# Kernel tuning notes

Measured on AMD Instinct MI355X. Metric: run time of the kernel, lower is better.

Reference implementation:

```python
import jax, jax.numpy as jnp
import numpy as np

H_GRU = 32  # GRU hidden size fixed to 32 in the module


def setup_inputs() -> dict:
    key = jax.random.key(0)
    ks = jax.random.split(key, 12)
    B, C_in, H, W = 64, 64, 48, 160
    C_out = 64
    s_in = 1.0 / np.sqrt(C_in)
    s_h = 1.0 / np.sqrt(H_GRU)
    u = lambda k, shape: jax.random.uniform(k, shape, jnp.float32, -s_h, s_h)
    return {
        "x": jax.random.normal(ks[0], (B, C_in, H, W), jnp.float32),
        "conv_w": jax.random.normal(ks[1], (C_out, C_in), jnp.float32) * s_in,
        "conv_b": jax.random.normal(ks[2], (C_out,), jnp.float32) * s_in,
        "wih_f": u(ks[3], (3 * H_GRU, C_out)),
        "whh_f": u(ks[4], (3 * H_GRU, H_GRU)),
        "bih_f": u(ks[5], (3 * H_GRU,)),
        "bhh_f": u(ks[6], (3 * H_GRU,)),
        "wih_b": u(ks[7], (3 * H_GRU, C_out)),
        "whh_b": u(ks[8], (3 * H_GRU, H_GRU)),
        "bih_b": u(ks[9], (3 * H_GRU,)),
        "bhh_b": u(ks[10], (3 * H_GRU,)),
    }


def _gru_scan(pre, whh, bhh):
    # pre: [N, T, 3H] input-side gate pre-activations (already x@Wih^T + bih)
    N = pre.shape[0]

    def step(h, g):
        gh = h @ whh.T + bhh
        gi_r, gi_z, gi_n = jnp.split(g, 3, axis=-1)
        gh_r, gh_z, gh_n = jnp.split(gh, 3, axis=-1)
        r = jax.nn.sigmoid(gi_r + gh_r)
        z = jax.nn.sigmoid(gi_z + gh_z)
        n = jnp.tanh(gi_n + r * gh_n)
        h_new = (1.0 - z) * n + z * h
        return h_new, h_new

    h0 = jnp.zeros((N, H_GRU), pre.dtype)
    _, ys = jax.lax.scan(step, h0, jnp.swapaxes(pre, 0, 1))  # ys: [T, N, H]
    return jnp.swapaxes(ys, 0, 1)  # [N, T, H]


def reference(x, conv_w, conv_b, wih_f, whh_f, bih_f, bhh_f,
              wih_b, whh_b, bih_b, bhh_b):
    B, C_in, H, W = x.shape
    # 1x1 conv fused with the NCHW->NHWC permute
    y = jnp.einsum('bchw,oc->bhwo', x, conv_w) + conv_b  # [B, H, W, C_out]
    C_out = y.shape[-1]
    seq = y.reshape(B * H, W, C_out)  # GRU batch = B*H, seq_len = W
    # forward direction
    pre_f = jnp.einsum('ntc,gc->ntg', seq, wih_f) + bih_f
    out_f = _gru_scan(pre_f, whh_f, bhh_f)
    # backward direction: scan reversed sequence, then flip output back
    seq_r = seq[:, ::-1, :]
    pre_b = jnp.einsum('ntc,gc->ntg', seq_r, wih_b) + bih_b
    out_b = _gru_scan(pre_b, whh_b, bhh_b)[:, ::-1, :]
    out = jnp.concatenate([out_f, out_b], axis=-1)  # [B*H, W, 2*H_GRU]
    out = out.reshape(B, H, W, 2 * H_GRU)
    return jnp.transpose(out, (0, 3, 1, 2))  # back to NCHW
```

## Files before the change

### kernel.cpp

```cpp
#include <hip/hip_runtime.h>


typedef _Float16 f16x8 __attribute__((ext_vector_type(8)));
typedef _Float16 f16x4 __attribute__((ext_vector_type(4)));
typedef __fp16   pk16  __attribute__((ext_vector_type(2)));
typedef float    f32x4 __attribute__((ext_vector_type(4)));

#define HWSTRIDE 7680
#define NW 10
#define WS_WHH2_OFF 24576
#define WS_BIAS_OFF 36864

__global__ void fold_weights(const float* __restrict__ conv_w,
                             const float* __restrict__ conv_b,
                             const float* __restrict__ wih_f,
                             const float* __restrict__ bih_f,
                             const float* __restrict__ bhh_f,
                             const float* __restrict__ wih_b,
                             const float* __restrict__ bih_b,
                             const float* __restrict__ bhh_b,
                             const float* __restrict__ whh_f,
                             const float* __restrict__ whh_b,
                             void* wsv)
{
    _Float16* W2   = (_Float16*)wsv;
    _Float16* whh2 = (_Float16*)((char*)wsv + WS_WHH2_OFF);
    float*    bias = (float*)((char*)wsv + WS_BIAS_OFF);
    const int idx = blockIdx.x * 256 + threadIdx.x;
    if (idx < 12288) {
        const int d = idx / 6144, r = idx % 6144, g = r / 64, c = r % 64;
        const float* wih = d ? wih_b : wih_f;
        float acc = 0.f;
        for (int o = 0; o < 64; ++o) acc += wih[g * 64 + o] * conv_w[o * 64 + c];
        W2[idx] = (_Float16)acc;
    } else if (idx < 18432) {
        const int e2 = idx - 12288;
        const int dd = e2 / 3072, rr = e2 % 3072, g = rr / 32, k = rr % 32;
        const int qq = k >> 3, ee = k & 7;
        const int jsrc = (ee < 4) ? (qq * 4 + ee) : (16 + qq * 4 + (ee - 4));
        const float* whh = dd ? whh_b : whh_f;
        whh2[e2] = (_Float16)whh[g * 32 + jsrc];
    } else if (idx < 18688) {
        const int e = idx - 18432;
        const int d = e >> 7, rr = e & 127, kind = rr >> 5, j = rr & 31;
        const float* wih = d ? wih_b : wih_f;
        const float* bih = d ? bih_b : bih_f;
        const float* bhh = d ? bhh_b : bhh_f;
        float v;
        if (kind == 0 || kind == 1) {
            const int g = j + kind * 32;
            float b2 = bih[g];
            for (int o = 0; o < 64; ++o) b2 += wih[g * 64 + o] * conv_b[o];
            v = b2 + bhh[g];
        } else if (kind == 2) {
            const int g = j + 64;
            float b2 = bih[g];
            for (int o = 0; o < 64; ++o) b2 += wih[g * 64 + o] * conv_b[o];
            v = b2;
        } else {
            v = bhh[j + 64];
        }
        bias[(d * 4 + kind) * 32 + j] = v;
    }
}

static __device__ __forceinline__ unsigned pkh(float a, float b) {
    pk16 p = __builtin_amdgcn_cvt_pkrtz(a, b);
    return __builtin_bit_cast(unsigned, p);
}

#define BAR() do { asm volatile("s_waitcnt lgkmcnt(0)" ::: "memory"); \
                   __builtin_amdgcn_s_barrier();                      \
                   asm volatile("" ::: "memory"); } while (0)

__global__ __launch_bounds__(256, 2)
void gru_fused7(const float* __restrict__ x,
                const void* __restrict__ wsv,
                float* __restrict__ out)
{
    __shared__ __align__(16) _Float16 xt[1024 * 16];
    __shared__ __align__(16) _Float16 spre[16 * 16 * 96];

    const int d    = blockIdx.x & 1;
    const int g2   = blockIdx.x >> 1;
    const int b    = g2 / 3;
    const int h0   = (g2 % 3) * 16;
    const int lane = threadIdx.x & 63;
    const int wave = threadIdx.x >> 6;
    const int sw   = blockIdx.x & 3;
    const int rel  = (wave - sw) & 3;
    const int q    = lane >> 4;
    const int s16  = lane & 15;

    const float* xb = x + (size_t)b * 64 * HWSTRIDE + (size_t)h0 * 160;

    if (rel != 0) {
        const int hw = rel - 1;
        const int u  = hw * 64 + lane;
        const int nq = (hw == 0) ? 22 : 21;

        const _Float16* W2 = (const _Float16*)wsv + (size_t)d * 96 * 64;
        f16x8 W2A[6][2];
        #pragma unroll
        for (int gt = 0; gt < 6; ++gt)
            #pragma unroll
            for (int kt = 0; kt < 2; ++kt)
                W2A[gt][kt] = *(const f16x8*)&W2[(gt * 16 + s16) * 64 + kt * 32 + q * 8];
        const float* bias = (const float*)((const char*)wsv + WS_BIAS_OFF) + d * 128;
        float biasC[6][4];
        #pragma unroll
        for (int gt = 0; gt < 6; ++gt)
            #pragma unroll
            for (int r = 0; r < 4; ++r)
                biasC[gt][r] = bias[(gt >> 1) * 32 + (gt & 1) * 16 + 4 * q + r];

        const int xsw = ((s16 >> 2) & 3) << 2;

        float4 pf[22];
        auto load_win = [&](int wi) {
            const int w0 = d ? (144 - 16 * wi) : (16 * wi);
            #pragma unroll
            for (int k = 0; k < 22; ++k) {
                if (k < nq) {
                    const int qd = u + 192 * k;
                    const int row = qd >> 2, m = qd & 3;
                    pf[k] = *(const float4*)(xb + (size_t)(row >> 4) * HWSTRIDE
                                             + (row & 15) * 160 + w0 + m * 4);
                }
            }
        };
        auto write_win = [&]() {
            #pragma unroll
            for (int k = 0; k < 22; ++k) {
                if (k < nq) {
                    const int qd = u + 192 * k;
                    const int row = qd >> 2, m = qd & 3;
                    const int wblk = (m * 4) ^ (((row >> 2) & 3) << 2);
                    uint2 v; v.x = pkh(pf[k].x, pf[k].y); v.y = pkh(pf[k].z, pf[k].w);
                    *(uint2*)&xt[row * 16 + wblk] = v;
                }
            }
        };
        auto project = [&]() {
            for (int tt = hw; tt < 16; tt += 3) {
                const int wl = d ? (15 - tt) : tt;
                const int wsel = wl ^ xsw;
                const int base0 = (q * 128 + s16) * 16 + wsel;
                f16x8 B0, B1;
                #pragma unroll
                for (int e = 0; e < 8; ++e) {
                    B0[e] = xt[base0 + e * 256];
                    B1[e] = xt[base0 + e * 256 + 8192];
                }
                #pragma unroll
                for (int gt = 0; gt < 6; ++gt) {
                    f32x4 acc = {biasC[gt][0], biasC[gt][1], biasC[gt][2], biasC[gt][3]};
                    acc = __builtin_amdgcn_mfma_f32_16x16x32_f16(W2A[gt][0], B0, acc, 0, 0, 0);
                    acc = __builtin_amdgcn_mfma_f32_16x16x32_f16(W2A[gt][1], B1, acc, 0, 0, 0);
                    uint2 v; v.x = pkh(acc[0], acc[1]); v.y = pkh(acc[2], acc[3]);
                    const int col = (gt * 16 + 4 * q) ^ ((s16 & 7) << 2);
                    *(uint2*)&spre[(tt * 16 + s16) * 96 + col] = v;
                }
            }
        };

        load_win(0);
        write_win();
        load_win(1);
        BAR();
        for (int i = 0; i < NW; ++i) {
            project();
            BAR();
            if (i + 1 < NW) {
                write_win();
                if (i + 2 < NW) load_win(i + 2);
            }
            BAR();
        }
    } else {
        const _Float16* whh2 = (const _Float16*)((const char*)wsv + WS_WHH2_OFF)
                               + (size_t)d * 96 * 32;
        f16x8 whhA[6];
        #pragma unroll
        for (int gt = 0; gt < 6; ++gt)
            whhA[gt] = *(const f16x8*)&whh2[(gt * 16 + s16) * 32 + q * 8];
        const float* bias = (const float*)((const char*)wsv + WS_BIAS_OFF) + d * 128;
        float bhN[2][4];
        #pragma unroll
        for (int jh = 0; jh < 2; ++jh)
            #pragma unroll
            for (int r = 0; r < 4; ++r)
                bhN[jh][r] = bias[96 + jh * 16 + 4 * q + r];

        float* ob = out + ((size_t)b * 64 + d * 32) * HWSTRIDE + (size_t)(h0 + s16) * 160;
        f16x8 hB = {};
        f16x8 hB16[16];
        float hprev[8];
        #pragma unroll
        for (int uu = 0; uu < 8; ++uu) hprev[uu] = 0.f;

        int spcol[6];
        #pragma unroll
        for (int gt = 0; gt < 6; ++gt)
            spcol[gt] = (gt * 16 + 4 * q) ^ ((s16 & 7) << 2);

        auto store_win = [&](int wi) {
            const int wbase = d ? (144 - 16 * wi) : (16 * wi);
            #pragma unroll
            for (int e = 0; e < 8; ++e) {
                const int j = (e >> 2) * 16 + 4 * q + (e & 3);
                float* pw = ob + (size_t)j * HWSTRIDE + wbase;
                #pragma unroll
                for (int m = 0; m < 4; ++m) {
                    float4 v;
                    if (d == 0)
                        v = make_float4((float)hB16[4*m][e],   (float)hB16[4*m+1][e],
                                        (float)hB16[4*m+2][e], (float)hB16[4*m+3][e]);
                    else
                        v = make_float4((float)hB16[15-4*m][e], (float)hB16[14-4*m][e],
                                        (float)hB16[13-4*m][e], (float)hB16[12-4*m][e]);
                    *(float4*)(pw + 4 * m) = v;
                }
            }
        };

        BAR();
        #pragma unroll 1
        for (int i = 0; i < NW; ++i) {
            if (i > 0) store_win(i - 1);
            BAR();
            f16x4 pg[4][6];
            #pragma unroll
            for (int tt = 0; tt < 16; ++tt) {
                if ((tt & 3) == 0) {
                    #pragma unroll
                    for (int t4 = 0; t4 < 4; ++t4)
                        #pragma unroll
                        for (int gt = 0; gt < 6; ++gt)
                            pg[t4][gt] = *(const f16x4*)
                                &spre[((tt + t4) * 16 + s16) * 96 + spcol[gt]];
                }
                const f16x4 p0 = pg[tt & 3][0], p1 = pg[tt & 3][1];
                const f16x4 p2 = pg[tt & 3][2], p3 = pg[tt & 3][3];
                const f16x4 p4 = pg[tt & 3][4], p5 = pg[tt & 3][5];
                f32x4 aR0 = {(float)p0[0], (float)p0[1], (float)p0[2], (float)p0[3]};
                f32x4 aR1 = {(float)p1[0], (float)p1[1], (float)p1[2], (float)p1[3]};
                f32x4 aZ0 = {(float)p2[0], (float)p2[1], (float)p2[2], (float)p2[3]};
                f32x4 aZ1 = {(float)p3[0], (float)p3[1], (float)p3[2], (float)p3[3]};
                f32x4 aN0 = {bhN[0][0], bhN[0][1], bhN[0][2], bhN[0][3]};
                f32x4 aN1 = {bhN[1][0], bhN[1][1], bhN[1][2], bhN[1][3]};
                aR0 = __builtin_amdgcn_mfma_f32_16x16x32_f16(whhA[0], hB, aR0, 0, 0, 0);
                aR1 = __builtin_amdgcn_mfma_f32_16x16x32_f16(whhA[1], hB, aR1, 0, 0, 0);
                aZ0 = __builtin_amdgcn_mfma_f32_16x16x32_f16(whhA[2], hB, aZ0, 0, 0, 0);
                aZ1 = __builtin_amdgcn_mfma_f32_16x16x32_f16(whhA[3], hB, aZ1, 0, 0, 0);
                aN0 = __builtin_amdgcn_mfma_f32_16x16x32_f16(whhA[4], hB, aN0, 0, 0, 0);
                aN1 = __builtin_amdgcn_mfma_f32_16x16x32_f16(whhA[5], hB, aN1, 0, 0, 0);
                float hn[8];
                #pragma unroll
                for (int r = 0; r < 4; ++r) {
                    const float rr = __builtin_amdgcn_rcpf(1.f + __expf(-aR0[r]));
                    const float zz = __builtin_amdgcn_rcpf(1.f + __expf(-aZ0[r]));
                    float ta = fmaf(rr, aN0[r], (float)p4[r]);
                    ta = fminf(fmaxf(ta, -15.f), 15.f);
                    const float e2 = __expf(2.f * ta);
                    const float nn = (e2 - 1.f) * __builtin_amdgcn_rcpf(e2 + 1.f);
                    hn[r] = (1.f - zz) * nn + zz * hprev[r];
                }
                #pragma unroll
                for (int r = 0; r < 4; ++r) {
                    const float rr = __builtin_amdgcn_rcpf(1.f + __expf(-aR1[r]));
                    const float zz = __builtin_amdgcn_rcpf(1.f + __expf(-aZ1[r]));
                    float ta = fmaf(rr, aN1[r], (float)p5[r]);
                    ta = fminf(fmaxf(ta, -15.f), 15.f);
                    const float e2 = __expf(2.f * ta);
                    const float nn = (e2 - 1.f) * __builtin_amdgcn_rcpf(e2 + 1.f);
                    hn[4 + r] = (1.f - zz) * nn + zz * hprev[4 + r];
                }
                {
                    uint4 hu;
                    hu.x = pkh(hn[0], hn[1]); hu.y = pkh(hn[2], hn[3]);
                    hu.z = pkh(hn[4], hn[5]); hu.w = pkh(hn[6], hn[7]);
                    hB = __builtin_bit_cast(f16x8, hu);
                }
                hB16[tt] = hB;
                #pragma unroll
                for (int uu = 0; uu < 8; ++uu) hprev[uu] = hn[uu];
            }
            BAR();
        }
        store_win(NW - 1);
    }
}

extern "C" void kernel_launch(void* const* d_in, const int* in_sizes, int n_in,
                              void* d_out, int out_size, void* d_ws, size_t ws_size,
                              hipStream_t stream) {
    (void)in_sizes; (void)n_in; (void)ws_size; (void)out_size;
    fold_weights<<<dim3(74), dim3(256), 0, stream>>>(
        (const float*)d_in[1],
        (const float*)d_in[2],
        (const float*)d_in[3],
        (const float*)d_in[5],
        (const float*)d_in[6],
        (const float*)d_in[7],
        (const float*)d_in[9],
        (const float*)d_in[10],
        (const float*)d_in[4],
        (const float*)d_in[8],
        d_ws);
    gru_fused7<<<dim3(384), dim3(256), 0, stream>>>(
        (const float*)d_in[0],
        d_ws,
        (float*)d_out);
}
```

Before: 214.6 us.

## Shrink GRU blocks to one producer wave with double-buffered 8-step windows

Each block drops from four waves to two: a single producer wave loads x, converts it to fp16 and computes input projections, while one recurrence wave runs the GRU. Time windows shrink from 16 to 8 steps (20 windows), the projection buffer is double-buffered so there is one barrier per window instead of two, and outputs are stored right after each window instead of lagging one window. Smaller blocks and LDS may let more blocks fit per CU. The cost is that the single producer wave must keep pace with the serial recurrence, the x swizzle is removed (possible LDS bank conflicts), and the register pressure of the 32-entry float4 prefetch.

```diff
diff --git a/kernel.cpp b/kernel.cpp
--- a/kernel.cpp
+++ b/kernel.cpp
@@ -7,7 +7,7 @@
 typedef float    f32x4 __attribute__((ext_vector_type(4)));
 
 #define HWSTRIDE 7680
-#define NW 10
+#define NW 20
 #define WS_WHH2_OFF 24576
 #define WS_BIAS_OFF 36864
 
@@ -73,32 +73,28 @@
                    __builtin_amdgcn_s_barrier();                      \
                    asm volatile("" ::: "memory"); } while (0)
 
-__global__ __launch_bounds__(256, 2)
-void gru_fused7(const float* __restrict__ x,
+__global__ __launch_bounds__(128, 1)
+void gru_fused8(const float* __restrict__ x,
                 const void* __restrict__ wsv,
                 float* __restrict__ out)
 {
-    __shared__ __align__(16) _Float16 xt[1024 * 16];
-    __shared__ __align__(16) _Float16 spre[16 * 16 * 96];
-
-    const int d    = blockIdx.x & 1;
-    const int g2   = blockIdx.x >> 1;
-    const int b    = g2 / 3;
-    const int h0   = (g2 % 3) * 16;
+    __shared__ __align__(16) _Float16 xt[1024 * 8];
+    __shared__ __align__(16) _Float16 spre[2 * 8 * 16 * 96];
+
+    const int bid  = blockIdx.x;
+    const int d    = bid / 192;
+    const int g    = bid % 192;
+    const int b    = g / 3;
+    const int h0   = (g % 3) * 16;
     const int lane = threadIdx.x & 63;
     const int wave = threadIdx.x >> 6;
-    const int sw   = blockIdx.x & 3;
-    const int rel  = (wave - sw) & 3;
+    const int sw   = bid & 1;
     const int q    = lane >> 4;
     const int s16  = lane & 15;
 
     const float* xb = x + (size_t)b * 64 * HWSTRIDE + (size_t)h0 * 160;
 
-    if (rel != 0) {
-        const int hw = rel - 1;
-        const int u  = hw * 64 + lane;
-        const int nq = (hw == 0) ? 22 : 21;
-
+    if (wave != sw) {
         const _Float16* W2 = (const _Float16*)wsv + (size_t)d * 96 * 64;
         f16x8 W2A[6][2];
         #pragma unroll
@@ -114,43 +110,39 @@
             for (int r = 0; r < 4; ++r)
                 biasC[gt][r] = bias[(gt >> 1) * 32 + (gt & 1) * 16 + 4 * q + r];
 
-        const int xsw = ((s16 >> 2) & 3) << 2;
-
-        float4 pf[22];
+        float4 pf[32];
         auto load_win = [&](int wi) {
-            const int w0 = d ? (144 - 16 * wi) : (16 * wi);
-            #pragma unroll
-            for (int k = 0; k < 22; ++k) {
-                if (k < nq) {
-                    const int qd = u + 192 * k;
-                    const int row = qd >> 2, m = qd & 3;
-                    pf[k] = *(const float4*)(xb + (size_t)(row >> 4) * HWSTRIDE
-                                             + (row & 15) * 160 + w0 + m * 4);
-                }
+            const int w0 = d ? (152 - 8 * wi) : (8 * wi);
+            #pragma unroll
+            for (int k = 0; k < 16; ++k) {
+                const int row = lane + 64 * k;
+                const float* p = xb + (size_t)(row >> 4) * HWSTRIDE + (row & 15) * 160 + w0;
+                pf[2 * k]     = *(const float4*)p;
+                pf[2 * k + 1] = *(const float4*)(p + 4);
             }
         };
-        auto write_win = [&]() {
-            #pragma unroll
-            for (int k = 0; k < 22; ++k) {
-                if (k < nq) {
-                    const int qd = u + 192 * k;
-                    const int row = qd >> 2, m = qd & 3;
-                    const int wblk = (m * 4) ^ (((row >> 2) & 3) << 2);
-                    uint2 v; v.x = pkh(pf[k].x, pf[k].y); v.y = pkh(pf[k].z, pf[k].w);
-                    *(uint2*)&xt[row * 16 + wblk] = v;
-                }
+        auto write_xt = [&]() {
+            #pragma unroll
+            for (int k = 0; k < 16; ++k) {
+                const int row = lane + 64 * k;
+                uint4 v;
+                v.x = pkh(pf[2*k].x,   pf[2*k].y);
+                v.y = pkh(pf[2*k].z,   pf[2*k].w);
+                v.z = pkh(pf[2*k+1].x, pf[2*k+1].y);
+                v.w = pkh(pf[2*k+1].z, pf[2*k+1].w);
+                *(uint4*)&xt[row * 8] = v;
             }
         };
-        auto project = [&]() {
-            for (int tt = hw; tt < 16; tt += 3) {
-                const int wl = d ? (15 - tt) : tt;
-                const int wsel = wl ^ xsw;
-                const int base0 = (q * 128 + s16) * 16 + wsel;
+        auto project = [&](int wi) {
+            _Float16* sp = &spre[(wi & 1) * 12288];
+            for (int tt = 0; tt < 8; ++tt) {
+                const int wl = d ? (7 - tt) : tt;
+                const int base0 = (q * 8) * 128 + s16 * 8 + wl;
                 f16x8 B0, B1;
                 #pragma unroll
                 for (int e = 0; e < 8; ++e) {
-                    B0[e] = xt[base0 + e * 256];
-                    B1[e] = xt[base0 + e * 256 + 8192];
+                    B0[e] = xt[base0 + e * 128];
+                    B1[e] = xt[base0 + e * 128 + 4096];
                 }
                 #pragma unroll
                 for (int gt = 0; gt < 6; ++gt) {
@@ -159,22 +151,17 @@
                     acc = __builtin_amdgcn_mfma_f32_16x16x32_f16(W2A[gt][1], B1, acc, 0, 0, 0);
                     uint2 v; v.x = pkh(acc[0], acc[1]); v.y = pkh(acc[2], acc[3]);
                     const int col = (gt * 16 + 4 * q) ^ ((s16 & 7) << 2);
-                    *(uint2*)&spre[(tt * 16 + s16) * 96 + col] = v;
+                    *(uint2*)&sp[(tt * 16 + s16) * 96 + col] = v;
                 }
             }
         };
 
         load_win(0);
-        write_win();
-        load_win(1);
-        BAR();
+        #pragma unroll 1
         for (int i = 0; i < NW; ++i) {
-            project();
-            BAR();
-            if (i + 1 < NW) {
-                write_win();
-                if (i + 2 < NW) load_win(i + 2);
-            }
+            write_xt();
+            project(i);
+            if (i + 1 < NW) load_win(i + 1);
             BAR();
         }
     } else {
@@ -194,7 +181,7 @@
 
         float* ob = out + ((size_t)b * 64 + d * 32) * HWSTRIDE + (size_t)(h0 + s16) * 160;
         f16x8 hB = {};
-        f16x8 hB16[16];
+        f16x8 hB8[8];
         float hprev[8];
         #pragma unroll
         for (int uu = 0; uu < 8; ++uu) hprev[uu] = 0.f;
@@ -204,41 +191,20 @@
         for (int gt = 0; gt < 6; ++gt)
             spcol[gt] = (gt * 16 + 4 * q) ^ ((s16 & 7) << 2);
 
-        auto store_win = [&](int wi) {
-            const int wbase = d ? (144 - 16 * wi) : (16 * wi);
-            #pragma unroll
-            for (int e = 0; e < 8; ++e) {
-                const int j = (e >> 2) * 16 + 4 * q + (e & 3);
-                float* pw = ob + (size_t)j * HWSTRIDE + wbase;
-                #pragma unroll
-                for (int m = 0; m < 4; ++m) {
-                    float4 v;
-                    if (d == 0)
-                        v = make_float4((float)hB16[4*m][e],   (float)hB16[4*m+1][e],
-                                        (float)hB16[4*m+2][e], (float)hB16[4*m+3][e]);
-                    else
-                        v = make_float4((float)hB16[15-4*m][e], (float)hB16[14-4*m][e],
-                                        (float)hB16[13-4*m][e], (float)hB16[12-4*m][e]);
-                    *(float4*)(pw + 4 * m) = v;
-                }
-            }
-        };
-
-        BAR();
         #pragma unroll 1
         for (int i = 0; i < NW; ++i) {
-            if (i > 0) store_win(i - 1);
             BAR();
+            const _Float16* sp = &spre[(i & 1) * 12288];
             f16x4 pg[4][6];
             #pragma unroll
-            for (int tt = 0; tt < 16; ++tt) {
+            for (int tt = 0; tt < 8; ++tt) {
                 if ((tt & 3) == 0) {
                     #pragma unroll
                     for (int t4 = 0; t4 < 4; ++t4)
                         #pragma unroll
                         for (int gt = 0; gt < 6; ++gt)
                             pg[t4][gt] = *(const f16x4*)
-                                &spre[((tt + t4) * 16 + s16) * 96 + spcol[gt]];
+                                &sp[((tt + t4) * 16 + s16) * 96 + spcol[gt]];
                 }
                 const f16x4 p0 = pg[tt & 3][0], p1 = pg[tt & 3][1];
                 const f16x4 p2 = pg[tt & 3][2], p3 = pg[tt & 3][3];
@@ -282,13 +248,30 @@
                     hu.z = pkh(hn[4], hn[5]); hu.w = pkh(hn[6], hn[7]);
                     hB = __builtin_bit_cast(f16x8, hu);
                 }
-                hB16[tt] = hB;
+                hB8[tt] = hB;
                 #pragma unroll
                 for (int uu = 0; uu < 8; ++uu) hprev[uu] = hn[uu];
             }
-            BAR();
+            {
+                const int w0 = d ? (152 - 8 * i) : (8 * i);
+                #pragma unroll
+                for (int e = 0; e < 8; ++e) {
+                    const int j = (e >> 2) * 16 + 4 * q + (e & 3);
+                    float* pw = ob + (size_t)j * HWSTRIDE + w0;
+                    if (d == 0) {
+                        *(float4*)(pw) = make_float4((float)hB8[0][e], (float)hB8[1][e],
+                                                     (float)hB8[2][e], (float)hB8[3][e]);
+                        *(float4*)(pw + 4) = make_float4((float)hB8[4][e], (float)hB8[5][e],
+                                                         (float)hB8[6][e], (float)hB8[7][e]);
+                    } else {
+                        *(float4*)(pw) = make_float4((float)hB8[7][e], (float)hB8[6][e],
+                                                     (float)hB8[5][e], (float)hB8[4][e]);
+                        *(float4*)(pw + 4) = make_float4((float)hB8[3][e], (float)hB8[2][e],
+                                                         (float)hB8[1][e], (float)hB8[0][e]);
+                    }
+                }
+            }
         }
-        store_win(NW - 1);
     }
 }
 
@@ -308,7 +291,7 @@
         (const float*)d_in[4],
         (const float*)d_in[8],
         d_ws);
-    gru_fused7<<<dim3(384), dim3(256), 0, stream>>>(
+    gru_fused8<<<dim3(384), dim3(128), 0, stream>>>(
         (const float*)d_in[0],
         d_ws,
         (float*)d_out);
```

Result: faster. 183.0 us (-14.7%).
